# Kernel optimization log

Hardware: AMD Instinct MI355X
Metric: run time of the kernel (lower is better)

Reference implementation:

```python
import jax, jax.numpy as jnp
import numpy as np
from jax import lax

SEQ, BATCH = 48, 12
D_A, D_V, D_T = 1582, 342, 1024
H = 300            # per-modality projection dim (hardcoded 300 in source)
G = 500            # g_hidden_size; 3*G == 1500 == fc1 in_features
NLAYERS = 64
NSPK, NCLASS = 9, 7
LAMDA, ALPHA = 0.5, 0.1   # hardcoded in my_GCN(...) call


def _lengths():
    # deterministic ragged dialogue lengths, max 48, sum == 411
    return 24 + (np.arange(BATCH) * 3) % 25


def setup_inputs() -> dict:
    key = jax.random.key(0)
    ks = jax.random.split(key, 12)
    lengths = _lengths()
    seq_idx = np.concatenate([np.arange(l) for l in lengths]).astype(np.int32)
    batch_idx = np.concatenate([np.full(l, j) for j, l in enumerate(lengths)]).astype(np.int32)
    s = 0.02
    return {
        "fea": jax.random.normal(ks[0], (SEQ, BATCH, D_T), jnp.float32),
        "speaker": jax.random.uniform(ks[1], (SEQ, BATCH, NSPK), jnp.float32),
        "fea_a": jax.random.normal(ks[2], (SEQ, BATCH, D_A), jnp.float32),
        "fea_v": jax.random.normal(ks[3], (SEQ, BATCH, D_V), jnp.float32),
        "fea_t": jax.random.normal(ks[4], (SEQ, BATCH, D_T), jnp.float32),
        "Wa": jax.random.normal(ks[5], (D_A, H), jnp.float32) * s,
        "ba": jnp.zeros((H,), jnp.float32),
        "Wv": jax.random.normal(ks[6], (D_V, H), jnp.float32) * s,
        "bv": jnp.zeros((H,), jnp.float32),
        "Wt": jax.random.normal(ks[7], (D_T, H), jnp.float32) * s,
        "bt": jnp.zeros((H,), jnp.float32),
        "spk_emb": jax.random.normal(ks[8], (NSPK, H), jnp.float32) * s,
        "W_in": jax.random.normal(ks[9], (H, G), jnp.float32) * s,
        "b_in": jnp.zeros((G,), jnp.float32),
        "W_convs": jax.random.normal(ks[10], (NLAYERS, 2 * G, G), jnp.float32) * s,
        "W_fc1": jax.random.normal(ks[11], (3 * G, NCLASS), jnp.float32) * s,
        "b_fc1": jnp.zeros((NCLASS,), jnp.float32),
        "utt_num": jnp.asarray(lengths, jnp.int32),
        "seq_idx": jnp.asarray(seq_idx),
        "batch_idx": jnp.asarray(batch_idx),
        "dia_id": jnp.asarray(batch_idx),
    }


def _arc_sim(c):
    # MMGCN similarity: 1 - arccos(0.99999*cos)/pi
    return 1.0 - jnp.arccos(jnp.clip(c * 0.99999, -1.0, 1.0)) / jnp.pi


def _forward(fea, speaker, fea_a, fea_v, fea_t, Wa, ba, Wv, bv, Wt, bt,
             spk_emb, W_in, b_in, W_convs, W_fc1, b_fc1,
             seq_idx, batch_idx, dia_id):
    # dense modality projections (fea itself is unused in the original forward)
    a = fea_a @ Wa + ba    # (S,B,H)
    v = fea_v @ Wv + bv
    t = fea_t @ Wt + bt

    # simple_batch_graphify: ragged gather of valid utterances -> (N,H)
    a_n = a[seq_idx, batch_idx]
    v_n = v[seq_idx, batch_idx]
    t_n = t[seq_idx, batch_idx]

    # speaker embedding added to text nodes (MMGCN convention)
    spk = jnp.argmax(speaker[seq_idx, batch_idx], axis=-1)
    t_n = t_n + spk_emb[spk]

    N = seq_idx.shape[0]
    feats = [a_n, v_n, t_n]
    fn = [f / (jnp.linalg.norm(f, axis=1, keepdims=True) + 1e-8) for f in feats]
    same_dia = (dia_id[:, None] == dia_id[None, :])  # block-diagonal mask

    # big adjacency over 3N nodes: intra-modal arccos-sim within a dialogue,
    # cross-modal diagonal links between same-utterance nodes
    blocks = []
    for m in range(3):
        row = []
        for n in range(3):
            if m == n:
                row.append(jnp.where(same_dia, _arc_sim(fn[m] @ fn[m].T), 0.0))
            else:
                d = _arc_sim(jnp.sum(fn[m] * fn[n], axis=1))
                row.append(jnp.diag(d))
        blocks.append(row)
    A = jnp.block(blocks)                       # (3N,3N)
    deg = A.sum(axis=1)
    dinv = jnp.where(deg > 0, deg ** -0.5, 0.0)
    A = A * dinv[:, None] * dinv[None, :]       # D^-1/2 A D^-1/2

    # 64-layer GCNII (variant=True): h_{l} = relu(theta_l*[A h, h0] W_l + (1-theta_l)*((1-a)Ah + a h0))
    x = jnp.concatenate(feats, axis=0)          # (3N,H)
    h0 = jax.nn.relu(x @ W_in + b_in)           # (3N,G)
    ls = jnp.arange(1, NLAYERS + 1, dtype=jnp.float32)

    def step(h, wl):
        W, l = wl
        theta = jnp.log(LAMDA / l + 1.0)
        hi = A @ h
        support = jnp.concatenate([hi, h0], axis=1)      # (3N,2G)
        r = (1.0 - ALPHA) * hi + ALPHA * h0
        return jax.nn.relu(theta * (support @ W) + (1.0 - theta) * r), None

    h, _ = lax.scan(step, h0, (W_convs, ls))

    # regroup per utterance: concat a/v/t node features -> (N, 3G=1500)
    feat = jnp.concatenate([h[:N], h[N:2 * N], h[2 * N:]], axis=1)
    logits = jax.nn.relu(feat) @ W_fc1 + b_fc1   # dropout is identity in eval
    return jax.nn.log_softmax(logits, axis=1)


def reference(fea, speaker, fea_a, fea_v, fea_t, Wa, ba, Wv, bv, Wt, bt,
              spk_emb, W_in, b_in, W_convs, W_fc1, b_fc1,
              utt_num, seq_idx, batch_idx, dia_id):
    return _forward(fea, speaker, fea_a, fea_v, fea_t, Wa, ba, Wv, bv, Wt, bt,
                    spk_emb, W_in, b_in, W_convs, W_fc1, b_fc1,
                    seq_idx, batch_idx, dia_id)
```

## Files before the change

### kernel.cpp

```cpp
#include <hip/hip_runtime.h>
#include <hip/hip_bf16.h>
#include <math.h>

#define LDA 1280
#define LDH 512
#define LDX 320

typedef __attribute__((ext_vector_type(8))) short short8;
typedef __attribute__((ext_vector_type(4))) float f32x4;

__device__ __forceinline__ unsigned short f2b(float x){
    unsigned int u = __float_as_uint(x);
    unsigned int r = (u + 0x7fffu + ((u >> 16) & 1u)) >> 16;
    return (unsigned short)r;
}
__device__ __forceinline__ float b2f(unsigned short u){
    return __uint_as_float(((unsigned int)u) << 16);
}

__device__ __forceinline__ float arc_sim(float c){
    float cc = c * 0.99999f;
    cc = fminf(1.f, fmaxf(-1.f, cc));
    return 1.f - acosf(cc) * 0.31830988618379067f;
}

__global__ __launch_bounds__(256)
void k_gather(const float* __restrict__ fa, const float* __restrict__ fv, const float* __restrict__ ft,
              const float* __restrict__ speaker, const int* __restrict__ seq, const int* __restrict__ bat,
              float* __restrict__ xga, float* __restrict__ xgv, float* __restrict__ xgt,
              int* __restrict__ spki, int N)
{
    int i = blockIdx.x;
    int tid = threadIdx.x;
    bool real = i < N;
    int s = real ? seq[i] : 0, b = real ? bat[i] : 0;
    size_t base = (size_t)(s*12 + b);
    for (int k = tid; k < 1600; k += 256) xga[(size_t)i*1600 + k] = (real && k < 1582) ? fa[base*1582 + k] : 0.f;
    for (int k = tid; k < 384;  k += 256) xgv[(size_t)i*384  + k] = (real && k < 342)  ? fv[base*342  + k] : 0.f;
    for (int k = tid; k < 1024; k += 256) xgt[(size_t)i*1024 + k] = real ? ft[base*1024 + k] : 0.f;
    if (tid == 0){
        int bi = 0;
        if (real){
            const float* sp = speaker + base*9;
            float best = sp[0];
            for (int c = 1; c < 9; ++c) if (sp[c] > best){ best = sp[c]; bi = c; }
        }
        spki[i] = bi;
    }
}

__global__ __launch_bounds__(256)
void k_trw(const float* __restrict__ W, int D, int Kp, float* __restrict__ WTr)
{
    __shared__ float tt[64][65];
    int k0 = blockIdx.x*64, j0 = blockIdx.y*64;
    int t = threadIdx.x;
    #pragma unroll
    for (int rr = 0; rr < 4; ++rr){
        int kl = (t >> 4) + rr*16;
        int k  = k0 + kl;
        int jl = (t & 15) * 4;
        int j  = j0 + jl;
        float4 v;
        if (k < D && j + 3 < 300){
            v = *(const float4*)&W[(size_t)k*300 + j];
        } else {
            v.x = (k < D && j+0 < 300) ? W[(size_t)k*300 + j+0] : 0.f;
            v.y = (k < D && j+1 < 300) ? W[(size_t)k*300 + j+1] : 0.f;
            v.z = (k < D && j+2 < 300) ? W[(size_t)k*300 + j+2] : 0.f;
            v.w = (k < D && j+3 < 300) ? W[(size_t)k*300 + j+3] : 0.f;
        }
        tt[jl+0][kl] = v.x; tt[jl+1][kl] = v.y; tt[jl+2][kl] = v.z; tt[jl+3][kl] = v.w;
    }
    __syncthreads();
    #pragma unroll
    for (int rr = 0; rr < 4; ++rr){
        int jl = (t >> 4) + rr*16;
        int j  = j0 + jl;
        int kq = (t & 15) * 4;
        if (j < 300){
            float4 o; o.x = tt[jl][kq]; o.y = tt[jl][kq+1]; o.z = tt[jl][kq+2]; o.w = tt[jl][kq+3];
            *(float4*)&WTr[(size_t)j*Kp + k0 + kq] = o;
        }
    }
}

__global__ __launch_bounds__(256)
void k_projg2(const float* __restrict__ xg, int Kp, int kslice,
              const float* __restrict__ WTr,
              float* __restrict__ xp)
{
    __shared__ float As[16][68];
    __shared__ float Bs[16][64];
    int i0 = blockIdx.y*64, j0 = blockIdx.x*64;
    int ks0 = blockIdx.z * kslice;
    int tid = threadIdx.x;
    int ty = tid >> 4, tx = tid & 15;
    int lr = tid >> 2, lk = (tid & 3) << 2;
    int bj = tid & 63, bk4 = (tid >> 6) << 2;
    float acc[4][4] = {};
    for (int k0 = 0; k0 < kslice; k0 += 16){
        float4 av = *(const float4*)&xg[(size_t)(i0+lr)*Kp + ks0 + k0 + lk];
        float4 wv = {0.f, 0.f, 0.f, 0.f};
        int j = j0 + bj;
        if (j < 300) wv = *(const float4*)&WTr[(size_t)j*Kp + ks0 + k0 + bk4];
        __syncthreads();
        As[lk+0][lr] = av.x; As[lk+1][lr] = av.y; As[lk+2][lr] = av.z; As[lk+3][lr] = av.w;
        Bs[bk4+0][bj] = wv.x; Bs[bk4+1][bj] = wv.y; Bs[bk4+2][bj] = wv.z; Bs[bk4+3][bj] = wv.w;
        __syncthreads();
        #pragma unroll
        for (int kk = 0; kk < 16; ++kk){
            float4 a4 = *(const float4*)&As[kk][ty*4];
            float4 b4 = *(const float4*)&Bs[kk][tx*4];
            float a_[4] = {a4.x, a4.y, a4.z, a4.w};
            float b_[4] = {b4.x, b4.y, b4.z, b4.w};
            #pragma unroll
            for (int u = 0; u < 4; ++u)
                #pragma unroll
                for (int v = 0; v < 4; ++v) acc[u][v] += a_[u]*b_[v];
        }
    }
    #pragma unroll
    for (int u = 0; u < 4; ++u){
        int i = i0 + ty*4 + u;
        #pragma unroll
        for (int v = 0; v < 4; ++v){
            int j = j0 + tx*4 + v;
            xp[((size_t)blockIdx.z*448 + i)*320 + j] = acc[u][v];
        }
    }
}

__global__ __launch_bounds__(256)
void k_norm2(const float* __restrict__ xpa, const float* __restrict__ xpv, const float* __restrict__ xpt,
             const float* __restrict__ ba, const float* __restrict__ bv, const float* __restrict__ bt,
             const float* __restrict__ spk_emb, const int* __restrict__ spki,
             float* __restrict__ x, float* __restrict__ fn, int N)
{
    __shared__ float red[4];
    int r = blockIdx.x, tid = threadIdx.x;
    int m = (r >= 2*N) ? 2 : (r >= N ? 1 : 0);
    int n = r - m*N;
    const float* xp   = (m==0) ? xpa : (m==1) ? xpv : xpt;
    const float* bias = (m==0) ? ba  : (m==1) ? bv  : bt;
    int KS = (m==1) ? 2 : 4;
    float v0 = 0.f, v1 = 0.f;
    int j0 = tid, j1 = tid + 256;
    if (j0 < 300){
        float s = bias[j0];
        for (int si = 0; si < KS; ++si) s += xp[((size_t)si*448 + n)*320 + j0];
        if (m == 2) s += spk_emb[spki[n]*300 + j0];
        v0 = s;
    }
    if (j1 < 300){
        float s = bias[j1];
        for (int si = 0; si < KS; ++si) s += xp[((size_t)si*448 + n)*320 + j1];
        if (m == 2) s += spk_emb[spki[n]*300 + j1];
        v1 = s;
    }
    float ss = v0*v0 + v1*v1;
    #pragma unroll
    for (int off = 32; off > 0; off >>= 1) ss += __shfl_down(ss, off, 64);
    if ((tid & 63) == 0) red[tid >> 6] = ss;
    __syncthreads();
    float tot = red[0] + red[1] + red[2] + red[3];
    float inv = 1.f / (sqrtf(tot) + 1e-8f);
    x [(size_t)r*LDX + j0] = v0;
    fn[(size_t)r*LDX + j0] = v0 * inv;
    if (j1 < 320){
        x [(size_t)r*LDX + j1] = v1;
        fn[(size_t)r*LDX + j1] = v1 * inv;
    }
}

__global__ __launch_bounds__(256)
void k_intra(const float* __restrict__ fn, const int* __restrict__ dia,
             float* __restrict__ A, int N)
{
    int m  = blockIdx.z;
    int i0 = blockIdx.y * 32, j0 = blockIdx.x * 32;
    int iend = min(i0 + 31, N - 1), jend = min(j0 + 31, N - 1);
    if (dia[iend] < dia[j0] || dia[jend] < dia[i0]) return;

    __shared__ float As[32][17], Bs[32][17];
    int tx = threadIdx.x, ty = threadIdx.y;
    int tid = ty*16 + tx;
    float acc[2][2] = {};
    for (int k0 = 0; k0 < 320; k0 += 16){
        __syncthreads();
        for (int l = tid; l < 512; l += 256){
            int r = l >> 4, kk = l & 15;
            int gi = i0 + r, gj = j0 + r;
            As[r][kk] = (gi < N) ? fn[((size_t)m*N + gi)*LDX + k0 + kk] : 0.f;
            Bs[r][kk] = (gj < N) ? fn[((size_t)m*N + gj)*LDX + k0 + kk] : 0.f;
        }
        __syncthreads();
        #pragma unroll
        for (int kk = 0; kk < 16; ++kk){
            float a0 = As[ty*2+0][kk], a1 = As[ty*2+1][kk];
            float b0 = Bs[tx*2+0][kk], b1 = Bs[tx*2+1][kk];
            acc[0][0] += a0*b0; acc[0][1] += a0*b1;
            acc[1][0] += a1*b0; acc[1][1] += a1*b1;
        }
    }
    #pragma unroll
    for (int u = 0; u < 2; ++u)
        #pragma unroll
        for (int v = 0; v < 2; ++v){
            int i = i0 + ty*2 + u, j = j0 + tx*2 + v;
            if (i < N && j < N){
                float val = (dia[i] == dia[j]) ? arc_sim(acc[u][v]) : 0.f;
                A[((size_t)m*N + i)*LDA + (size_t)m*N + j] = val;
            }
        }
}

__global__ void k_cross(const float* __restrict__ fn, float* __restrict__ A, int N)
{
    int i = blockIdx.x, lane = threadIdx.x;
    float d01 = 0.f, d02 = 0.f, d12 = 0.f;
    for (int k = lane; k < 300; k += 64){
        float a = fn[((size_t)0*N + i)*LDX + k];
        float b = fn[((size_t)1*N + i)*LDX + k];
        float c = fn[((size_t)2*N + i)*LDX + k];
        d01 += a*b; d02 += a*c; d12 += b*c;
    }
    #pragma unroll
    for (int off = 32; off > 0; off >>= 1){
        d01 += __shfl_down(d01, off, 64);
        d02 += __shfl_down(d02, off, 64);
        d12 += __shfl_down(d12, off, 64);
    }
    if (lane == 0){
        float s01 = arc_sim(d01), s02 = arc_sim(d02), s12 = arc_sim(d12);
        size_t r0 = i, r1 = (size_t)N + i, r2 = (size_t)2*N + i;
        A[r0*LDA + r1] = s01; A[r1*LDA + r0] = s01;
        A[r0*LDA + r2] = s02; A[r2*LDA + r0] = s02;
        A[r1*LDA + r2] = s12; A[r2*LDA + r1] = s12;
    }
}

__global__ __launch_bounds__(256)
void k_rowsum(const float* __restrict__ A, float* __restrict__ dinv, int M3)
{
    __shared__ float red[4];
    int r = blockIdx.x, tid = threadIdx.x;
    float s = 0.f;
    for (int c = tid; c < M3; c += 256) s += A[(size_t)r*LDA + c];
    #pragma unroll
    for (int off = 32; off > 0; off >>= 1) s += __shfl_down(s, off, 64);
    if ((tid & 63) == 0) red[tid >> 6] = s;
    __syncthreads();
    if (tid == 0){
        float tot = red[0] + red[1] + red[2] + red[3];
        dinv[r] = (tot > 0.f) ? 1.f / sqrtf(tot) : 0.f;
    }
}

__global__ void k_scale(float* __restrict__ A, unsigned short* __restrict__ Abf,
                        const float* __restrict__ dinv, int M3)
{
    int c = blockIdx.x*16 + threadIdx.x;
    int r = blockIdx.y*16 + threadIdx.y;
    if (r < M3 && c < M3){
        float v = A[(size_t)r*LDA + c] * dinv[r]*dinv[c];
        A[(size_t)r*LDA + c] = v;
        Abf[(size_t)r*LDA + c] = f2b(v);
    }
}

__global__ __launch_bounds__(256)
void k_gemm_h0(const float* __restrict__ x, const float* __restrict__ Win,
               const float* __restrict__ bin, float* __restrict__ h0,
               unsigned short* __restrict__ h0b, unsigned short* __restrict__ h0bT, int M3)
{
    __shared__ float As[16][68];
    __shared__ float Bs[16][64];
    int i0 = blockIdx.y*64, j0 = blockIdx.x*64;
    int tid = threadIdx.x;
    int ty = tid >> 4, tx = tid & 15;
    int lr = tid >> 2, lk = (tid & 3) << 2;
    int br = tid >> 4, bc = (tid & 15) << 2;
    float acc[4][4] = {};
    for (int k0 = 0; k0 < 320; k0 += 16){
        float4 av = *(const float4*)&x[(size_t)(i0+lr)*LDX + k0 + lk];
        float4 bwv;
        {
            int kr = k0 + br;
            int c0 = j0 + bc;
            if (kr < 300 && c0 + 3 < 500){
                bwv = *(const float4*)&Win[(size_t)kr*500 + c0];
            } else {
                bwv.x = (kr < 300 && c0+0 < 500) ? Win[(size_t)kr*500 + c0+0] : 0.f;
                bwv.y = (kr < 300 && c0+1 < 500) ? Win[(size_t)kr*500 + c0+1] : 0.f;
                bwv.z = (kr < 300 && c0+2 < 500) ? Win[(size_t)kr*500 + c0+2] : 0.f;
                bwv.w = (kr < 300 && c0+3 < 500) ? Win[(size_t)kr*500 + c0+3] : 0.f;
            }
        }
        __syncthreads();
        As[lk+0][lr] = av.x; As[lk+1][lr] = av.y; As[lk+2][lr] = av.z; As[lk+3][lr] = av.w;
        *(float4*)&Bs[br][bc] = bwv;
        __syncthreads();
        #pragma unroll
        for (int kk = 0; kk < 16; ++kk){
            float4 a4 = *(const float4*)&As[kk][ty*4];
            float4 b4 = *(const float4*)&Bs[kk][tx*4];
            float a_[4] = {a4.x, a4.y, a4.z, a4.w};
            float b_[4] = {b4.x, b4.y, b4.z, b4.w};
            #pragma unroll
            for (int u = 0; u < 4; ++u)
                #pragma unroll
                for (int v = 0; v < 4; ++v) acc[u][v] += a_[u]*b_[v];
        }
    }
    #pragma unroll
    for (int u = 0; u < 4; ++u){
        int i = i0 + ty*4 + u;
        #pragma unroll
        for (int v = 0; v < 4; ++v){
            int j = j0 + tx*4 + v;
            float val = 0.f;
            if (i < M3 && j < 500){
                val = fmaxf(acc[u][v] + bin[j], 0.f);
            }
            h0[(size_t)i*LDH + j] = val;
            unsigned short bv = f2b(val);
            h0b[(size_t)i*LDH + j] = bv;
            h0bT[(size_t)j*LDA + i] = bv;
        }
    }
}

__global__ __launch_bounds__(256)
void k_wtr(const float* __restrict__ Wc, int g, unsigned short* __restrict__ Wt)
{
    __shared__ unsigned short sT[64][72];
    int l = g*8 + blockIdx.z;
    int slot = l & 7;
    int k0 = blockIdx.x*64, j0 = blockIdx.y*64;
    const float* W = Wc + (size_t)l*1000*500;
    int ksrc0 = (k0 < 512) ? k0 : k0 - 12;
    int klim  = (k0 < 512) ? 500 : 1000;
    int t = threadIdx.x;
    #pragma unroll
    for (int rr = 0; rr < 4; ++rr){
        int kl = (t >> 4) + rr*16;
        int k  = ksrc0 + kl;
        int jl = (t & 15) * 4;
        int j  = j0 + jl;
        bool vk = (k < klim);
        float4 v;
        if (vk && j + 3 < 500){
            v = *(const float4*)&W[(size_t)k*500 + j];
        } else {
            v.x = (vk && j+0 < 500) ? W[(size_t)k*500 + j+0] : 0.f;
            v.y = (vk && j+1 < 500) ? W[(size_t)k*500 + j+1] : 0.f;
            v.z = (vk && j+2 < 500) ? W[(size_t)k*500 + j+2] : 0.f;
            v.w = (vk && j+3 < 500) ? W[(size_t)k*500 + j+3] : 0.f;
        }
        sT[jl+0][kl] = f2b(v.x);
        sT[jl+1][kl] = f2b(v.y);
        sT[jl+2][kl] = f2b(v.z);
        sT[jl+3][kl] = f2b(v.w);
    }
    __syncthreads();
    int jl = t >> 2, kc = (t & 3) * 16;
    unsigned short* dst = Wt + (size_t)slot*LDH*1024 + (size_t)(j0+jl)*1024 + k0 + kc;
    *(uint4*)&dst[0] = *(const uint4*)&sT[jl][kc];
    *(uint4*)&dst[8] = *(const uint4*)&sT[jl][kc+8];
}

#define SWZ(r, k) (((r)*64 + (k)) ^ (((r)&7)<<3))

__global__ __launch_bounds__(256)
void k_spmm(const unsigned short* __restrict__ Abf, const unsigned short* __restrict__ hT,
            float* __restrict__ hi, unsigned short* __restrict__ hib)
{
    __shared__ unsigned short sA[64*64], sB[64*64];
    const int i0 = blockIdx.y*64, j0 = blockIdx.x*64;
    const int tid = threadIdx.x, lane = tid & 63, w = tid >> 6;
    const int wr = w >> 1, wc = w & 1;
    const int srow = tid >> 2, scol = (tid & 3) * 16;
    const unsigned short* pa = &Abf[(size_t)(i0+srow)*LDA + scol];
    const unsigned short* pb = &hT [(size_t)(j0+srow)*LDA + scol];
    uint4 a0 = *(const uint4*)(pa);
    uint4 a1 = *(const uint4*)(pa + 8);
    uint4 b0 = *(const uint4*)(pb);
    uint4 b1 = *(const uint4*)(pb + 8);
    f32x4 acc[2][2] = {};
    for (int k0 = 0; k0 < 1280; k0 += 64){
        *(uint4*)&sA[SWZ(srow, scol)]     = a0;
        *(uint4*)&sA[SWZ(srow, scol + 8)] = a1;
        *(uint4*)&sB[SWZ(srow, scol)]     = b0;
        *(uint4*)&sB[SWZ(srow, scol + 8)] = b1;
        if (k0 + 64 < 1280){
            a0 = *(const uint4*)(pa + k0 + 64);
            a1 = *(const uint4*)(pa + k0 + 72);
            b0 = *(const uint4*)(pb + k0 + 64);
            b1 = *(const uint4*)(pb + k0 + 72);
        }
        __syncthreads();
        #pragma unroll
        for (int ks = 0; ks < 2; ++ks){
            int kk = ks*32 + (lane >> 4)*8;
            short8 af[2], bfr[2];
            #pragma unroll
            for (int fr = 0; fr < 2; ++fr){
                int r = wr*32 + fr*16 + (lane & 15);
                af[fr] = *(const short8*)&sA[SWZ(r, kk)];
            }
            #pragma unroll
            for (int fc = 0; fc < 2; ++fc){
                int c = wc*32 + fc*16 + (lane & 15);
                bfr[fc] = *(const short8*)&sB[SWZ(c, kk)];
            }
            #pragma unroll
            for (int fr = 0; fr < 2; ++fr)
                #pragma unroll
                for (int fc = 0; fc < 2; ++fc)
                    acc[fr][fc] = __builtin_amdgcn_mfma_f32_16x16x32_bf16(af[fr], bfr[fc], acc[fr][fc], 0, 0, 0);
        }
        __syncthreads();
    }
    #pragma unroll
    for (int fr = 0; fr < 2; ++fr)
        #pragma unroll
        for (int fc = 0; fc < 2; ++fc)
            #pragma unroll
            for (int rg = 0; rg < 4; ++rg){
                int i = i0 + wr*32 + fr*16 + (lane >> 4)*4 + rg;
                int j = j0 + wc*32 + fc*16 + (lane & 15);
                float v = acc[fr][fc][rg];
                hi [(size_t)i*LDH + j] = v;
                hib[(size_t)i*LDH + j] = f2b(v);
            }
}

__global__ __launch_bounds__(256)
void k_layerm(const unsigned short* __restrict__ hib, const unsigned short* __restrict__ h0b,
              const unsigned short* __restrict__ Wt, const float* __restrict__ hi,
              const float* __restrict__ h0, float theta, float cth,
              unsigned short* __restrict__ hT_out)
{
    __shared__ unsigned short sA[64*64], sB[64*64];
    const int i0 = blockIdx.y*64, j0 = blockIdx.x*64;
    const int tid = threadIdx.x, lane = tid & 63, w = tid >> 6;
    const int wr = w >> 1, wc = w & 1;
    const int srow = tid >> 2, scol = (tid & 3) * 16;
    const unsigned short* pa0 = &hib[(size_t)(i0+srow)*LDH + scol];
    const unsigned short* pa1 = &h0b[(size_t)(i0+srow)*LDH + scol];
    const unsigned short* pw  = &Wt [(size_t)(j0+srow)*1024 + scol];
    uint4 a0 = *(const uint4*)(pa0);
    uint4 a1 = *(const uint4*)(pa0 + 8);
    uint4 b0 = *(const uint4*)(pw);
    uint4 b1 = *(const uint4*)(pw + 8);
    f32x4 acc[2][2] = {};
    for (int k0 = 0; k0 < 1024; k0 += 64){
        *(uint4*)&sA[SWZ(srow, scol)]     = a0;
        *(uint4*)&sA[SWZ(srow, scol + 8)] = a1;
        *(uint4*)&sB[SWZ(srow, scol)]     = b0;
        *(uint4*)&sB[SWZ(srow, scol + 8)] = b1;
        int kn = k0 + 64;
        if (kn < 1024){
            const unsigned short* ap = (kn < 512) ? (pa0 + kn) : (pa1 + kn - 512);
            a0 = *(const uint4*)(ap);
            a1 = *(const uint4*)(ap + 8);
            b0 = *(const uint4*)(pw + kn);
            b1 = *(const uint4*)(pw + kn + 8);
        }
        __syncthreads();
        #pragma unroll
        for (int ks = 0; ks < 2; ++ks){
            int kk = ks*32 + (lane >> 4)*8;
            short8 af[2], bfr[2];
            #pragma unroll
            for (int fr = 0; fr < 2; ++fr){
                int r = wr*32 + fr*16 + (lane & 15);
                af[fr] = *(const short8*)&sA[SWZ(r, kk)];
            }
            #pragma unroll
            for (int fc = 0; fc < 2; ++fc){
                int c = wc*32 + fc*16 + (lane & 15);
                bfr[fc] = *(const short8*)&sB[SWZ(c, kk)];
            }
            #pragma unroll
            for (int fr = 0; fr < 2; ++fr)
                #pragma unroll
                for (int fc = 0; fc < 2; ++fc)
                    acc[fr][fc] = __builtin_amdgcn_mfma_f32_16x16x32_bf16(af[fr], bfr[fc], acc[fr][fc], 0, 0, 0);
        }
        __syncthreads();
    }
    #pragma unroll
    for (int fr = 0; fr < 2; ++fr)
        #pragma unroll
        for (int fc = 0; fc < 2; ++fc)
            #pragma unroll
            for (int rg = 0; rg < 4; ++rg){
                int i = i0 + wr*32 + fr*16 + (lane >> 4)*4 + rg;
                int j = j0 + wc*32 + fc*16 + (lane & 15);
                float hv  = hi[(size_t)i*LDH + j];
                float h0v = h0[(size_t)i*LDH + j];
                float o = fmaxf(theta*acc[fr][fc][rg] + cth*(0.9f*hv + 0.1f*h0v), 0.f);
                hT_out[(size_t)j*LDA + i] = f2b(o);
            }
}

__global__ void k_final(const unsigned short* __restrict__ hT, const float* __restrict__ Wfc,
                        const float* __restrict__ bfc, float* __restrict__ out, int N)
{
    int i = blockIdx.x, lane = threadIdx.x;
    float acc[7] = {};
    for (int k = lane; k < 1500; k += 64){
        int m = (k >= 1000) ? 2 : ((k >= 500) ? 1 : 0);
        int kk = k - m*500;
        float f = b2f(hT[(size_t)kk*LDA + m*N + i]);
        f = fmaxf(f, 0.f);
        #pragma unroll
        for (int c = 0; c < 7; ++c) acc[c] += f * Wfc[(size_t)k*7 + c];
    }
    #pragma unroll
    for (int off = 32; off > 0; off >>= 1){
        #pragma unroll
        for (int c = 0; c < 7; ++c) acc[c] += __shfl_down(acc[c], off, 64);
    }
    if (lane == 0){
        float lg[7], mx = -1e30f;
        #pragma unroll
        for (int c = 0; c < 7; ++c){ lg[c] = acc[c] + bfc[c]; mx = fmaxf(mx, lg[c]); }
        float s = 0.f;
        #pragma unroll
        for (int c = 0; c < 7; ++c) s += expf(lg[c] - mx);
        float lse = mx + logf(s);
        #pragma unroll
        for (int c = 0; c < 7; ++c) out[(size_t)i*7 + c] = lg[c] - lse;
    }
}

extern "C" void kernel_launch(void* const* d_in, const int* in_sizes, int n_in,
                              void* d_out, int out_size, void* d_ws, size_t ws_size,
                              hipStream_t stream)
{
    const float* speaker = (const float*)d_in[1];
    const float* fea_a   = (const float*)d_in[2];
    const float* fea_v   = (const float*)d_in[3];
    const float* fea_t   = (const float*)d_in[4];
    const float* Wa      = (const float*)d_in[5];
    const float* ba      = (const float*)d_in[6];
    const float* Wv      = (const float*)d_in[7];
    const float* bv      = (const float*)d_in[8];
    const float* Wt_in   = (const float*)d_in[9];
    const float* bt      = (const float*)d_in[10];
    const float* spk_emb = (const float*)d_in[11];
    const float* W_in    = (const float*)d_in[12];
    const float* b_in    = (const float*)d_in[13];
    const float* W_convs = (const float*)d_in[14];
    const float* W_fc1   = (const float*)d_in[15];
    const float* b_fc1   = (const float*)d_in[16];
    const int* seq = (const int*)d_in[18];
    const int* bat = (const int*)d_in[19];
    const int* dia = (const int*)d_in[20];

    const int N  = in_sizes[18];
    const int M3 = 3*N;

    char* wsb = (char*)d_ws;
    float*          Aw   = (float*)(wsb);
    unsigned short* Abf  = (unsigned short*)(wsb + 6553600);
    float*          x    = (float*)(wsb + 9830400);
    float*          fn   = (float*)(wsb + 11468800);
    float*          h0   = (float*)(wsb + 13107200);
    unsigned short* h0b  = (unsigned short*)(wsb + 15728640);
    unsigned short* h0bT = (unsigned short*)(wsb + 17039360);
    unsigned short* hTa  = (unsigned short*)(wsb + 18350080);
    unsigned short* hTb  = (unsigned short*)(wsb + 19660800);
    float*          hi   = (float*)(wsb + 20971520);
    unsigned short* hib  = (unsigned short*)(wsb + 23592960);
    unsigned short* Wt   = (unsigned short*)(wsb + 24903680);
    float*          dinv = (float*)(wsb + 33292288);
    float*          xga  = (float*)(wsb + 33297408);
    float*          xgv  = (float*)(wsb + 36164608);
    float*          xgt  = (float*)(wsb + 36852736);
    int*            spki = (int*)(wsb + 38687744);
    float*          WaT  = (float*)(wsb + 20971520);
    float*          WvT  = (float*)(wsb + 22891520);
    float*          WtT  = (float*)(wsb + 23352320);
    float*          xpa  = (float*)(wsb + 24581120);
    float*          xpv  = (float*)(wsb + 26874880);
    float*          xpt  = (float*)(wsb + 28021760);

    hipMemsetAsync(Aw,  0, 6553600, stream);
    hipMemsetAsync(Abf, 0, 3276800, stream);
    hipMemsetAsync(x,   0, 1638400, stream);
    hipMemsetAsync(fn,  0, 1638400, stream);

    k_gather<<<448, 256, 0, stream>>>(fea_a, fea_v, fea_t, speaker, seq, bat, xga, xgv, xgt, spki, N);

    k_trw<<<dim3(25, 5), 256, 0, stream>>>(Wa,    1582, 1600, WaT);
    k_trw<<<dim3( 6, 5), 256, 0, stream>>>(Wv,     342,  384, WvT);
    k_trw<<<dim3(16, 5), 256, 0, stream>>>(Wt_in, 1024, 1024, WtT);

    k_projg2<<<dim3(5, 7, 4), 256, 0, stream>>>(xga, 1600, 400, WaT, xpa);
    k_projg2<<<dim3(5, 7, 2), 256, 0, stream>>>(xgv,  384, 192, WvT, xpv);
    k_projg2<<<dim3(5, 7, 4), 256, 0, stream>>>(xgt, 1024, 256, WtT, xpt);

    k_norm2<<<M3, 256, 0, stream>>>(xpa, xpv, xpt, ba, bv, bt, spk_emb, spki, x, fn, N);

    int nt = (N + 31)/32;
    k_intra<<<dim3(nt, nt, 3), dim3(16,16), 0, stream>>>(fn, dia, Aw, N);
    k_cross<<<N, 64, 0, stream>>>(fn, Aw, N);
    k_rowsum<<<M3, 256, 0, stream>>>(Aw, dinv, M3);
    k_scale<<<dim3((M3+15)/16, (M3+15)/16), dim3(16,16), 0, stream>>>(Aw, Abf, dinv, M3);

    k_gemm_h0<<<dim3(8, 20), 256, 0, stream>>>(x, W_in, b_in, h0, h0b, h0bT, M3);

    const unsigned short* curT = h0bT;
    unsigned short* pp[2] = {hTa, hTb};
    for (int l = 1; l <= 64; ++l){
        if (((l-1) & 7) == 0)
            k_wtr<<<dim3(16, 8, 8), 256, 0, stream>>>(W_convs, (l-1) >> 3, Wt);
        k_spmm<<<dim3(8, 20), 256, 0, stream>>>(Abf, curT, hi, hib);
        float th = logf(0.5f/(float)l + 1.0f);
        unsigned short* o = pp[(l-1) & 1];
        k_layerm<<<dim3(8, 20), 256, 0, stream>>>(hib, h0b, Wt + (size_t)((l-1) & 7)*LDH*1024,
                                                  hi, h0, th, 1.0f - th, o);
        curT = o;
    }

    k_final<<<N, 64, 0, stream>>>(curT, W_fc1, b_fc1, (float*)d_out, N);
}
```

Before: 1.340 ms.

## Fuse all GCN layers into one persistent kernel with grid barriers

Replaces the 64-layer loop of separate spmm and layer-GEMM launches, plus the batched weight-transpose launches, with a single persistent kernel of 160 blocks. The blocks synchronise through an atomic-counter grid barrier. The bf16 conversion of the next layer's weights is overlapped with the current layer's spmm using a double-buffered weight slot. This removes roughly 130 kernel launches and their gaps. In exchange it depends on all 160 blocks being co-resident, and spin-wait barriers are added between phases.

```diff
diff --git a/kernel.cpp b/kernel.cpp
--- a/kernel.cpp
+++ b/kernel.cpp
@@ -5,6 +5,7 @@
 #define LDA 1280
 #define LDH 512
 #define LDX 320
+#define NB  160
 
 typedef __attribute__((ext_vector_type(8))) short short8;
 typedef __attribute__((ext_vector_type(4))) float f32x4;
@@ -22,6 +23,17 @@
     float cc = c * 0.99999f;
     cc = fminf(1.f, fmaxf(-1.f, cc));
     return 1.f - acosf(cc) * 0.31830988618379067f;
+}
+
+__device__ __forceinline__ void gbar(int* bar, int target){
+    __syncthreads();
+    if (threadIdx.x == 0){
+        __threadfence();
+        __hip_atomic_fetch_add(bar, 1, __ATOMIC_ACQ_REL, __HIP_MEMORY_SCOPE_AGENT);
+        while (__hip_atomic_load(bar, __ATOMIC_ACQUIRE, __HIP_MEMORY_SCOPE_AGENT) < target)
+            __builtin_amdgcn_s_sleep(2);
+    }
+    __syncthreads();
 }
 
 __global__ __launch_bounds__(256)
@@ -331,14 +343,14 @@
     }
 }
 
-__global__ __launch_bounds__(256)
-void k_wtr(const float* __restrict__ Wc, int g, unsigned short* __restrict__ Wt)
-{
-    __shared__ unsigned short sT[64][72];
-    int l = g*8 + blockIdx.z;
-    int slot = l & 7;
-    int k0 = blockIdx.x*64, j0 = blockIdx.y*64;
-    const float* W = Wc + (size_t)l*1000*500;
+#define SWZ(r, k) (((r)*64 + (k)) ^ (((r)&7)<<3))
+
+__device__ __forceinline__ void convW(const float* __restrict__ W, unsigned short* __restrict__ dstSlot,
+                                      void* smemv, int bid)
+{
+    unsigned short (*sT)[72] = (unsigned short (*)[72])smemv;
+    int jt = bid >> 4, kt = bid & 15;
+    int k0 = kt*64, j0 = jt*64;
     int ksrc0 = (k0 < 512) ? k0 : k0 - 12;
     int klim  = (k0 < 512) ? 500 : 1000;
     int t = threadIdx.x;
@@ -365,145 +377,157 @@
     }
     __syncthreads();
     int jl = t >> 2, kc = (t & 3) * 16;
-    unsigned short* dst = Wt + (size_t)slot*LDH*1024 + (size_t)(j0+jl)*1024 + k0 + kc;
+    unsigned short* dst = dstSlot + (size_t)(j0+jl)*1024 + k0 + kc;
     *(uint4*)&dst[0] = *(const uint4*)&sT[jl][kc];
     *(uint4*)&dst[8] = *(const uint4*)&sT[jl][kc+8];
 }
 
-#define SWZ(r, k) (((r)*64 + (k)) ^ (((r)&7)<<3))
-
-__global__ __launch_bounds__(256)
-void k_spmm(const unsigned short* __restrict__ Abf, const unsigned short* __restrict__ hT,
-            float* __restrict__ hi, unsigned short* __restrict__ hib)
-{
-    __shared__ unsigned short sA[64*64], sB[64*64];
-    const int i0 = blockIdx.y*64, j0 = blockIdx.x*64;
+__global__ __launch_bounds__(256)
+void k_layers(const unsigned short* __restrict__ Abf,
+              const unsigned short* __restrict__ h0bT,
+              const unsigned short* __restrict__ h0b,
+              const float* __restrict__ h0,
+              const float* __restrict__ Wc,
+              float* __restrict__ hi, unsigned short* __restrict__ hib,
+              unsigned short* __restrict__ hTa, unsigned short* __restrict__ hTb,
+              unsigned short* __restrict__ Wslot,
+              int* __restrict__ bar)
+{
+    __shared__ __align__(16) char smem[16896];
+    unsigned short* sA = (unsigned short*)smem;
+    unsigned short* sB = (unsigned short*)(smem + 8192);
+
+    const int bid = blockIdx.x;
     const int tid = threadIdx.x, lane = tid & 63, w = tid >> 6;
     const int wr = w >> 1, wc = w & 1;
     const int srow = tid >> 2, scol = (tid & 3) * 16;
-    const unsigned short* pa = &Abf[(size_t)(i0+srow)*LDA + scol];
-    const unsigned short* pb = &hT [(size_t)(j0+srow)*LDA + scol];
-    uint4 a0 = *(const uint4*)(pa);
-    uint4 a1 = *(const uint4*)(pa + 8);
-    uint4 b0 = *(const uint4*)(pb);
-    uint4 b1 = *(const uint4*)(pb + 8);
-    f32x4 acc[2][2] = {};
-    for (int k0 = 0; k0 < 1280; k0 += 64){
-        *(uint4*)&sA[SWZ(srow, scol)]     = a0;
-        *(uint4*)&sA[SWZ(srow, scol + 8)] = a1;
-        *(uint4*)&sB[SWZ(srow, scol)]     = b0;
-        *(uint4*)&sB[SWZ(srow, scol + 8)] = b1;
-        if (k0 + 64 < 1280){
-            a0 = *(const uint4*)(pa + k0 + 64);
-            a1 = *(const uint4*)(pa + k0 + 72);
-            b0 = *(const uint4*)(pb + k0 + 64);
-            b1 = *(const uint4*)(pb + k0 + 72);
-        }
-        __syncthreads();
-        #pragma unroll
-        for (int ks = 0; ks < 2; ++ks){
-            int kk = ks*32 + (lane >> 4)*8;
-            short8 af[2], bfr[2];
-            #pragma unroll
-            for (int fr = 0; fr < 2; ++fr){
-                int r = wr*32 + fr*16 + (lane & 15);
-                af[fr] = *(const short8*)&sA[SWZ(r, kk)];
-            }
-            #pragma unroll
-            for (int fc = 0; fc < 2; ++fc){
-                int c = wc*32 + fc*16 + (lane & 15);
-                bfr[fc] = *(const short8*)&sB[SWZ(c, kk)];
+    const int i0 = (bid >> 3) * 64, j0 = (bid & 7) * 64;
+    int target = NB;
+
+    if (bid < 128) convW(Wc, Wslot, smem, bid);
+    gbar(bar, target); target += NB;
+
+    const unsigned short* curT = h0bT;
+    for (int l = 1; l <= 64; ++l){
+        {
+            const unsigned short* pa = &Abf[(size_t)(i0+srow)*LDA + scol];
+            const unsigned short* pb = &curT[(size_t)(j0+srow)*LDA + scol];
+            uint4 a0 = *(const uint4*)(pa);
+            uint4 a1 = *(const uint4*)(pa + 8);
+            uint4 b0 = *(const uint4*)(pb);
+            uint4 b1 = *(const uint4*)(pb + 8);
+            f32x4 acc[2][2] = {};
+            for (int k0 = 0; k0 < 1280; k0 += 64){
+                *(uint4*)&sA[SWZ(srow, scol)]     = a0;
+                *(uint4*)&sA[SWZ(srow, scol + 8)] = a1;
+                *(uint4*)&sB[SWZ(srow, scol)]     = b0;
+                *(uint4*)&sB[SWZ(srow, scol + 8)] = b1;
+                if (k0 + 64 < 1280){
+                    a0 = *(const uint4*)(pa + k0 + 64);
+                    a1 = *(const uint4*)(pa + k0 + 72);
+                    b0 = *(const uint4*)(pb + k0 + 64);
+                    b1 = *(const uint4*)(pb + k0 + 72);
+                }
+                __syncthreads();
+                #pragma unroll
+                for (int ks = 0; ks < 2; ++ks){
+                    int kk = ks*32 + (lane >> 4)*8;
+                    short8 af[2], bfr[2];
+                    #pragma unroll
+                    for (int fr = 0; fr < 2; ++fr)
+                        af[fr] = *(const short8*)&sA[SWZ(wr*32 + fr*16 + (lane & 15), kk)];
+                    #pragma unroll
+                    for (int fc = 0; fc < 2; ++fc)
+                        bfr[fc] = *(const short8*)&sB[SWZ(wc*32 + fc*16 + (lane & 15), kk)];
+                    #pragma unroll
+                    for (int fr = 0; fr < 2; ++fr)
+                        #pragma unroll
+                        for (int fc = 0; fc < 2; ++fc)
+                            acc[fr][fc] = __builtin_amdgcn_mfma_f32_16x16x32_bf16(af[fr], bfr[fc], acc[fr][fc], 0, 0, 0);
+                }
+                __syncthreads();
             }
             #pragma unroll
             for (int fr = 0; fr < 2; ++fr)
                 #pragma unroll
                 for (int fc = 0; fc < 2; ++fc)
-                    acc[fr][fc] = __builtin_amdgcn_mfma_f32_16x16x32_bf16(af[fr], bfr[fc], acc[fr][fc], 0, 0, 0);
-        }
-        __syncthreads();
-    }
-    #pragma unroll
-    for (int fr = 0; fr < 2; ++fr)
-        #pragma unroll
-        for (int fc = 0; fc < 2; ++fc)
-            #pragma unroll
-            for (int rg = 0; rg < 4; ++rg){
-                int i = i0 + wr*32 + fr*16 + (lane >> 4)*4 + rg;
-                int j = j0 + wc*32 + fc*16 + (lane & 15);
-                float v = acc[fr][fc][rg];
-                hi [(size_t)i*LDH + j] = v;
-                hib[(size_t)i*LDH + j] = f2b(v);
+                    #pragma unroll
+                    for (int rg = 0; rg < 4; ++rg){
+                        int i = i0 + wr*32 + fr*16 + (lane >> 4)*4 + rg;
+                        int j = j0 + wc*32 + fc*16 + (lane & 15);
+                        float v = acc[fr][fc][rg];
+                        hi [(size_t)i*LDH + j] = v;
+                        hib[(size_t)i*LDH + j] = f2b(v);
+                    }
+        }
+        if (l < 64 && bid < 128){
+            __syncthreads();
+            convW(Wc + (size_t)l*500000, Wslot + (size_t)(l & 1)*LDH*1024, smem, bid);
+        }
+        gbar(bar, target); target += NB;
+
+        {
+            const unsigned short* Wl = Wslot + (size_t)((l-1) & 1)*LDH*1024;
+            float th = logf(0.5f/(float)l + 1.0f);
+            float cth = 1.0f - th;
+            const unsigned short* pa0 = &hib[(size_t)(i0+srow)*LDH + scol];
+            const unsigned short* pa1 = &h0b[(size_t)(i0+srow)*LDH + scol];
+            const unsigned short* pw  = &Wl [(size_t)(j0+srow)*1024 + scol];
+            uint4 a0 = *(const uint4*)(pa0);
+            uint4 a1 = *(const uint4*)(pa0 + 8);
+            uint4 b0 = *(const uint4*)(pw);
+            uint4 b1 = *(const uint4*)(pw + 8);
+            f32x4 acc[2][2] = {};
+            for (int k0 = 0; k0 < 1024; k0 += 64){
+                *(uint4*)&sA[SWZ(srow, scol)]     = a0;
+                *(uint4*)&sA[SWZ(srow, scol + 8)] = a1;
+                *(uint4*)&sB[SWZ(srow, scol)]     = b0;
+                *(uint4*)&sB[SWZ(srow, scol + 8)] = b1;
+                int kn = k0 + 64;
+                if (kn < 1024){
+                    const unsigned short* ap = (kn < 512) ? (pa0 + kn) : (pa1 + kn - 512);
+                    a0 = *(const uint4*)(ap);
+                    a1 = *(const uint4*)(ap + 8);
+                    b0 = *(const uint4*)(pw + kn);
+                    b1 = *(const uint4*)(pw + kn + 8);
+                }
+                __syncthreads();
+                #pragma unroll
+                for (int ks = 0; ks < 2; ++ks){
+                    int kk = ks*32 + (lane >> 4)*8;
+                    short8 af[2], bfr[2];
+                    #pragma unroll
+                    for (int fr = 0; fr < 2; ++fr)
+                        af[fr] = *(const short8*)&sA[SWZ(wr*32 + fr*16 + (lane & 15), kk)];
+                    #pragma unroll
+                    for (int fc = 0; fc < 2; ++fc)
+                        bfr[fc] = *(const short8*)&sB[SWZ(wc*32 + fc*16 + (lane & 15), kk)];
+                    #pragma unroll
+                    for (int fr = 0; fr < 2; ++fr)
+                        #pragma unroll
+                        for (int fc = 0; fc < 2; ++fc)
+                            acc[fr][fc] = __builtin_amdgcn_mfma_f32_16x16x32_bf16(af[fr], bfr[fc], acc[fr][fc], 0, 0, 0);
+                }
+                __syncthreads();
             }
-}
-
-__global__ __launch_bounds__(256)
-void k_layerm(const unsigned short* __restrict__ hib, const unsigned short* __restrict__ h0b,
-              const unsigned short* __restrict__ Wt, const float* __restrict__ hi,
-              const float* __restrict__ h0, float theta, float cth,
-              unsigned short* __restrict__ hT_out)
-{
-    __shared__ unsigned short sA[64*64], sB[64*64];
-    const int i0 = blockIdx.y*64, j0 = blockIdx.x*64;
-    const int tid = threadIdx.x, lane = tid & 63, w = tid >> 6;
-    const int wr = w >> 1, wc = w & 1;
-    const int srow = tid >> 2, scol = (tid & 3) * 16;
-    const unsigned short* pa0 = &hib[(size_t)(i0+srow)*LDH + scol];
-    const unsigned short* pa1 = &h0b[(size_t)(i0+srow)*LDH + scol];
-    const unsigned short* pw  = &Wt [(size_t)(j0+srow)*1024 + scol];
-    uint4 a0 = *(const uint4*)(pa0);
-    uint4 a1 = *(const uint4*)(pa0 + 8);
-    uint4 b0 = *(const uint4*)(pw);
-    uint4 b1 = *(const uint4*)(pw + 8);
-    f32x4 acc[2][2] = {};
-    for (int k0 = 0; k0 < 1024; k0 += 64){
-        *(uint4*)&sA[SWZ(srow, scol)]     = a0;
-        *(uint4*)&sA[SWZ(srow, scol + 8)] = a1;
-        *(uint4*)&sB[SWZ(srow, scol)]     = b0;
-        *(uint4*)&sB[SWZ(srow, scol + 8)] = b1;
-        int kn = k0 + 64;
-        if (kn < 1024){
-            const unsigned short* ap = (kn < 512) ? (pa0 + kn) : (pa1 + kn - 512);
-            a0 = *(const uint4*)(ap);
-            a1 = *(const uint4*)(ap + 8);
-            b0 = *(const uint4*)(pw + kn);
-            b1 = *(const uint4*)(pw + kn + 8);
-        }
-        __syncthreads();
-        #pragma unroll
-        for (int ks = 0; ks < 2; ++ks){
-            int kk = ks*32 + (lane >> 4)*8;
-            short8 af[2], bfr[2];
-            #pragma unroll
-            for (int fr = 0; fr < 2; ++fr){
-                int r = wr*32 + fr*16 + (lane & 15);
-                af[fr] = *(const short8*)&sA[SWZ(r, kk)];
-            }
-            #pragma unroll
-            for (int fc = 0; fc < 2; ++fc){
-                int c = wc*32 + fc*16 + (lane & 15);
-                bfr[fc] = *(const short8*)&sB[SWZ(c, kk)];
-            }
+            unsigned short* out = ((l-1) & 1) ? hTb : hTa;
             #pragma unroll
             for (int fr = 0; fr < 2; ++fr)
                 #pragma unroll
                 for (int fc = 0; fc < 2; ++fc)
-                    acc[fr][fc] = __builtin_amdgcn_mfma_f32_16x16x32_bf16(af[fr], bfr[fc], acc[fr][fc], 0, 0, 0);
-        }
-        __syncthreads();
-    }
-    #pragma unroll
-    for (int fr = 0; fr < 2; ++fr)
-        #pragma unroll
-        for (int fc = 0; fc < 2; ++fc)
-            #pragma unroll
-            for (int rg = 0; rg < 4; ++rg){
-                int i = i0 + wr*32 + fr*16 + (lane >> 4)*4 + rg;
-                int j = j0 + wc*32 + fc*16 + (lane & 15);
-                float hv  = hi[(size_t)i*LDH + j];
-                float h0v = h0[(size_t)i*LDH + j];
-                float o = fmaxf(theta*acc[fr][fc][rg] + cth*(0.9f*hv + 0.1f*h0v), 0.f);
-                hT_out[(size_t)j*LDA + i] = f2b(o);
-            }
+                    #pragma unroll
+                    for (int rg = 0; rg < 4; ++rg){
+                        int i = i0 + wr*32 + fr*16 + (lane >> 4)*4 + rg;
+                        int j = j0 + wc*32 + fc*16 + (lane & 15);
+                        float hv  = hi[(size_t)i*LDH + j];
+                        float h0v = h0[(size_t)i*LDH + j];
+                        float o = fmaxf(th*acc[fr][fc][rg] + cth*(0.9f*hv + 0.1f*h0v), 0.f);
+                        out[(size_t)j*LDA + i] = f2b(o);
+                    }
+            curT = out;
+        }
+        if (l < 64){ gbar(bar, target); target += NB; }
+    }
 }
 
 __global__ void k_final(const unsigned short* __restrict__ hT, const float* __restrict__ Wfc,
@@ -576,8 +600,9 @@
     unsigned short* hTb  = (unsigned short*)(wsb + 19660800);
     float*          hi   = (float*)(wsb + 20971520);
     unsigned short* hib  = (unsigned short*)(wsb + 23592960);
-    unsigned short* Wt   = (unsigned short*)(wsb + 24903680);
+    unsigned short* Wslot= (unsigned short*)(wsb + 24903680);
     float*          dinv = (float*)(wsb + 33292288);
+    int*            bar  = (int*)(wsb + 33297408 - 128);
     float*          xga  = (float*)(wsb + 33297408);
     float*          xgv  = (float*)(wsb + 36164608);
     float*          xgt  = (float*)(wsb + 36852736);
@@ -585,14 +610,15 @@
     float*          WaT  = (float*)(wsb + 20971520);
     float*          WvT  = (float*)(wsb + 22891520);
     float*          WtT  = (float*)(wsb + 23352320);
-    float*          xpa  = (float*)(wsb + 24581120);
-    float*          xpv  = (float*)(wsb + 26874880);
-    float*          xpt  = (float*)(wsb + 28021760);
+    float*          xpa  = (float*)(wsb + 24903680 + 2097152);
+    float*          xpv  = (float*)(wsb + 24903680 + 2097152 + 2293760);
+    float*          xpt  = (float*)(wsb + 24903680 + 2097152 + 2293760 + 1146880);
 
     hipMemsetAsync(Aw,  0, 6553600, stream);
     hipMemsetAsync(Abf, 0, 3276800, stream);
     hipMemsetAsync(x,   0, 1638400, stream);
     hipMemsetAsync(fn,  0, 1638400, stream);
+    hipMemsetAsync(bar, 0, 4,       stream);
 
     k_gather<<<448, 256, 0, stream>>>(fea_a, fea_v, fea_t, speaker, seq, bat, xga, xgv, xgt, spki, N);
 
@@ -614,18 +640,7 @@
 
     k_gemm_h0<<<dim3(8, 20), 256, 0, stream>>>(x, W_in, b_in, h0, h0b, h0bT, M3);
 
-    const unsigned short* curT = h0bT;
-    unsigned short* pp[2] = {hTa, hTb};
-    for (int l = 1; l <= 64; ++l){
-        if (((l-1) & 7) == 0)
-            k_wtr<<<dim3(16, 8, 8), 256, 0, stream>>>(W_convs, (l-1) >> 3, Wt);
-        k_spmm<<<dim3(8, 20), 256, 0, stream>>>(Abf, curT, hi, hib);
-        float th = logf(0.5f/(float)l + 1.0f);
-        unsigned short* o = pp[(l-1) & 1];
-        k_layerm<<<dim3(8, 20), 256, 0, stream>>>(hib, h0b, Wt + (size_t)((l-1) & 7)*LDH*1024,
-                                                  hi, h0, th, 1.0f - th, o);
-        curT = o;
-    }
-
-    k_final<<<N, 64, 0, stream>>>(curT, W_fc1, b_fc1, (float*)d_out, N);
-}
+    k_layers<<<NB, 256, 0, stream>>>(Abf, h0bT, h0b, h0, W_convs, hi, hib, hTa, hTb, Wslot, bar);
+
+    k_final<<<N, 64, 0, stream>>>(hTb, W_fc1, b_fc1, (float*)d_out, N);
+}
```

After: 2.790 ms. +108.3%, slower.
